# Kernel tuning notes

Hardware: AMD Instinct MI355X
Metric: run time of the kernel (lower is better)

Reference implementation:

```python
import jax, jax.numpy as jnp
import numpy as np

B = 262144
L, NO, NW = 5, 5, 3          # num_layers, num_ops, num_widths
AD = L * NO * NW             # arch_dim = 75
D, H = 64, 4                 # embed_dim, num_heads
HD = D // H                  # head_dim = 16
EPS = 1e-5


def _ln(x, g, b):
    m = x.mean(-1, keepdims=True)
    v = ((x - m) ** 2).mean(-1, keepdims=True)
    return (x - m) / jnp.sqrt(v + EPS) * g + b


def setup_inputs() -> dict:
    key = jax.random.key(0)
    ks = jax.random.split(key, 16)
    s = 0.05
    return {
        "hw_idx": jax.random.randint(ks[0], (B,), 0, 4),
        "op_indices": jax.random.randint(ks[1], (B, L), 0, NO),
        "width_indices": jax.random.randint(ks[2], (B, L), 0, NW),
        "hw_embed": jax.random.normal(ks[3], (4, D)) * s,
        "W1": jax.random.normal(ks[4], (128, AD)) * s, "b1": jnp.zeros((128,)),
        "W2": jax.random.normal(ks[5], (D, 128)) * s, "b2": jnp.zeros((D,)),
        "ln1_g": jnp.ones((D,)), "ln1_b": jnp.zeros((D,)),
        "in_proj_w": jax.random.normal(ks[6], (3 * D, D)) * s,
        "in_proj_b": jnp.zeros((3 * D,)),
        "out_proj_w": jax.random.normal(ks[7], (D, D)) * s,
        "out_proj_b": jnp.zeros((D,)),
        "ln2_g": jnp.ones((D,)), "ln2_b": jnp.zeros((D,)),
        "W3": jax.random.normal(ks[8], (32, D)) * s, "b3": jnp.zeros((32,)),
        "W4": jax.random.normal(ks[9], (1, 32)) * s, "b4": jnp.zeros((1,)),
    }


def reference(hw_idx, op_indices, width_indices, hw_embed, W1, b1, W2, b2,
              ln1_g, ln1_b, in_proj_w, in_proj_b, out_proj_w, out_proj_b,
              ln2_g, ln2_b, W3, b3, W4, b4):
    # hardware embedding lookup -> [B, D]
    hw_emb = hw_embed[hw_idx]
    # vectorized one-hot arch encoding: [B, L*NO*NW]
    cell = op_indices * NW + width_indices                  # [B, L]
    onehot = jax.nn.one_hot(cell, NO * NW, dtype=jnp.float32).reshape(-1, AD)
    # arch encoder MLP + LayerNorm (dropout = identity at eval)
    h = jax.nn.relu(onehot @ W1.T + b1)
    arch_emb = _ln(h @ W2.T + b2, ln1_g, ln1_b)             # [B, D]
    # combined sequence of 2 tokens: [B, 2, D]
    combined = jnp.stack([hw_emb, arch_emb], axis=1)
    # multi-head self-attention (torch MultiheadAttention, batch_first)
    qkv = combined @ in_proj_w.T + in_proj_b                # [B, 2, 3D]
    q, k, v = jnp.split(qkv, 3, axis=-1)
    q = q.reshape(-1, 2, H, HD); k = k.reshape(-1, 2, H, HD); v = v.reshape(-1, 2, H, HD)
    scores = jnp.einsum('bqhd,bkhd->bhqk', q, k) / np.sqrt(HD)
    attn = jax.nn.softmax(scores, axis=-1)
    ctx = jnp.einsum('bhqk,bkhd->bqhd', attn, v).reshape(-1, 2, D)
    attn_out = ctx @ out_proj_w.T + out_proj_b
    # residual + LayerNorm, mean-pool over the 2 tokens
    x = _ln(attn_out + combined, ln2_g, ln2_b)
    pooled = x.mean(axis=1)                                 # [B, D]
    # prediction head
    latency = jax.nn.relu(pooled @ W3.T + b3) @ W4.T + b4   # [B, 1]
    return latency
```

## Files before the change

kernel.cpp:

```cpp
#include <hip/hip_runtime.h>


using s8v = __attribute__((ext_vector_type(8))) short;
using h8  = __attribute__((ext_vector_type(8))) _Float16;
using h2v = __attribute__((ext_vector_type(2))) _Float16;
using f4  = __attribute__((ext_vector_type(4))) float;

#define WF_W1   0
#define WF_W2   12288
#define WF_IP   20480
#define WF_OP   32768
#define WF_W3   36864
#define WF_HWE  38912
#define TQ0     39168
#define TK0     39424
#define TV0B    39680
#define TV0R    39936
#define TBQ     40192

#define PWS     3456

__device__ __forceinline__ unsigned short f2h(float f) {
  _Float16 h = (_Float16)f;
  return __builtin_bit_cast(unsigned short, h);
}

__device__ __forceinline__ float dot8(h8 a, h8 b, float acc) {
  const f4 af = __builtin_bit_cast(f4, a), bf = __builtin_bit_cast(f4, b);
#pragma unroll
  for (int u = 0; u < 4; ++u)
    acc = __builtin_amdgcn_fdot2(__builtin_bit_cast(h2v, af[u]),
                                 __builtin_bit_cast(h2v, bf[u]), acc, false);
  return acc;
}

__device__ __forceinline__ void swz(const float* __restrict__ W,
                                    const float* __restrict__ bias,
                                    unsigned short* __restrict__ dst,
                                    int Kreal, int KS, int NT, int t, int stride) {
  const int total = KS * NT * 512;
  for (int i = t; i < total; i += stride) {
    const int j = i & 7, ln = (i >> 3) & 63, fr = i >> 9;
    const int nt = fr % NT, ks = fr / NT;
    const int n = nt * 16 + (ln & 15);
    const int k = ks * 32 + (ln >> 4) * 8 + j;
    float v = 0.f;
    if (k < Kreal) v = W[n * Kreal + k];
    else if (bias && k == Kreal) v = bias[n];
    dst[i] = f2h(v);
  }
}

__global__ void k_pre(const float* __restrict__ hwe,
                      const float* __restrict__ W1, const float* __restrict__ b1,
                      const float* __restrict__ W2,
                      const float* __restrict__ ipw, const float* __restrict__ ipb,
                      const float* __restrict__ opw,
                      const float* __restrict__ W3,
                      unsigned short* __restrict__ ws) {
  const int t = blockIdx.x * 256 + threadIdx.x;
  const int stride = gridDim.x * 256;
  swz(W1,  b1,      ws + WF_W1, 75, 3, 8, t, stride);
  swz(W2,  nullptr, ws + WF_W2, 128, 4, 4, t, stride);
  swz(ipw, nullptr, ws + WF_IP, 64, 2, 12, t, stride);
  swz(opw, nullptr, ws + WF_OP, 64, 2, 4, t, stride);
  swz(W3,  nullptr, ws + WF_W3, 64, 2, 2, t, stride);
  for (int i = t; i < 256; i += stride) ws[WF_HWE + i] = f2h(hwe[i]);
  for (int i = t; i < 768; i += stride) {
    const int hw = i / 192, n = i - hw * 192;
    const float* er = hwe + hw * 64;
    const float* wr = ipw + (size_t)n * 64;
    float acc = 0.f;
#pragma unroll 8
    for (int d = 0; d < 64; ++d) acc += er[d] * wr[d];
    if (n < 64)       ws[TQ0  + hw * 64 + n]         = f2h(acc + ipb[n]);
    else if (n < 128) ws[TK0  + hw * 64 + (n - 64)]  = f2h(acc);
    else {            ws[TV0B + hw * 64 + (n - 128)] = f2h(acc + ipb[n]);
                      ws[TV0R + hw * 64 + (n - 128)] = f2h(acc); }
  }
  for (int i = t; i < 64; i += stride) ws[TBQ + i] = f2h(ipb[i]);
}

__global__ __launch_bounds__(256, 4) void k_fused(
    const int* __restrict__ g_hw,
    const int* __restrict__ g_op, const int* __restrict__ g_wd,
    const float* __restrict__ g_hwe,
    const float* __restrict__ g_b2,
    const float* __restrict__ g_ln1g, const float* __restrict__ g_ln1b,
    const float* __restrict__ g_opb,
    const float* __restrict__ g_ln2g, const float* __restrict__ g_ln2b,
    const float* __restrict__ g_b3,  const float* __restrict__ g_W4,
    const float* __restrict__ g_b4,
    const unsigned short* __restrict__ wsf,
    float* __restrict__ g_out) {
  __shared__ __align__(16) unsigned short sm[4 * PWS];
  const int tid = threadIdx.x;
  const int wave = tid >> 6, lane = tid & 63;
  const int quad = lane >> 4, l15 = lane & 15;
  unsigned short* pw = sm + wave * PWS;
  const int m0 = (blockIdx.x * 4 + wave) * 16;

  int hwv = 0, c0 = 0, c1 = 0, c2 = 0, c3 = 0, c4 = 0;
  if (lane < 16) {
    const int smp = m0 + lane;
    hwv = g_hw[smp];
    c0 =      g_op[smp * 5 + 0] * 3 + g_wd[smp * 5 + 0];
    c1 = 15 + g_op[smp * 5 + 1] * 3 + g_wd[smp * 5 + 1];
    c2 = 30 + g_op[smp * 5 + 2] * 3 + g_wd[smp * 5 + 2];
    c3 = 45 + g_op[smp * 5 + 3] * 3 + g_wd[smp * 5 + 3];
    c4 = 60 + g_op[smp * 5 + 4] * 3 + g_wd[smp * 5 + 4];
  }
  const int t0 = __shfl(c0, l15), t1 = __shfl(c1, l15), t2 = __shfl(c2, l15);
  const int t3 = __shfl(c3, l15), t4 = __shfl(c4, l15);
  const int hwrow = __shfl(hwv, l15);

  float b2v[4], l1gv[4], l1bv[4], opbv[4], l2gv[4], l2bv[4];
#pragma unroll
  for (int nt = 0; nt < 4; ++nt) {
    const int col = nt * 16 + l15;
    b2v[nt] = g_b2[col];  l1gv[nt] = g_ln1g[col]; l1bv[nt] = g_ln1b[col];
    opbv[nt] = g_opb[col]; l2gv[nt] = g_ln2g[col]; l2bv[nt] = g_ln2b[col];
  }
  float b3v[2], w4vv[2];
#pragma unroll
  for (int nt = 0; nt < 2; ++nt) {
    b3v[nt] = g_b3[nt * 16 + l15];
    w4vv[nt] = g_W4[nt * 16 + l15];
  }
  const float b4v = g_b4[0];

  unsigned w0 = (1u << t0) | (1u << t1);
  unsigned w1 = 1u << (t3 - 32);
  unsigned w2 = 1u << 11;
  {
    const unsigned m2 = 1u << (t2 & 31);
    w0 |= (t2 < 32) ? m2 : 0u;
    w1 |= (t2 >= 32) ? m2 : 0u;
    const unsigned m4 = 1u << (t4 & 31);
    w1 |= (t4 < 64) ? m4 : 0u;
    w2 |= (t4 >= 64) ? m4 : 0u;
  }
  h8 aoh[3];
#pragma unroll
  for (int ks = 0; ks < 3; ++ks) {
    const unsigned wm = (ks == 0) ? w0 : (ks == 1) ? w1 : w2;
    const unsigned sh = wm >> (quad * 8);
    s8v a;
#pragma unroll
    for (int j = 0; j < 8; ++j)
      a[j] = ((sh >> j) & 1u) ? (short)0x3C00 : (short)0;
    aoh[ks] = __builtin_bit_cast(h8, a);
  }

#pragma unroll
  for (int half = 0; half < 2; ++half) {
    h8 bf[12];
#pragma unroll
    for (int n2 = 0; n2 < 4; ++n2)
#pragma unroll
      for (int ks = 0; ks < 3; ++ks)
        bf[n2 * 3 + ks] = *(const h8*)(wsf + WF_W1 +
            ((ks * 8 + half * 4 + n2) * 64 + lane) * 8);
#pragma unroll
    for (int n2 = 0; n2 < 4; ++n2) {
      f4 acc = {0.f, 0.f, 0.f, 0.f};
#pragma unroll
      for (int ks = 0; ks < 3; ++ks)
        acc = __builtin_amdgcn_mfma_f32_16x16x32_f16(aoh[ks], bf[n2 * 3 + ks],
                                                     acc, 0, 0, 0);
      const int col = (half * 4 + n2) * 16 + l15;
#pragma unroll
      for (int r = 0; r < 4; ++r) {
        float v = acc[r];
        v = v > 0.f ? v : 0.f;
        pw[(quad * 4 + r) * 136 + col] = f2h(v);
      }
    }
  }

  h8 a2[4];
#pragma unroll
  for (int ks = 0; ks < 4; ++ks)
    a2[ks] = *(const h8*)(pw + l15 * 136 + ks * 32 + quad * 8);
  float archres[4][4];
  {
    float val[4][4];
#pragma unroll
    for (int half = 0; half < 2; ++half) {
      h8 bf[8];
#pragma unroll
      for (int n2 = 0; n2 < 2; ++n2)
#pragma unroll
        for (int ks = 0; ks < 4; ++ks)
          bf[n2 * 4 + ks] = *(const h8*)(wsf + WF_W2 +
              ((ks * 4 + half * 2 + n2) * 64 + lane) * 8);
#pragma unroll
      for (int n2 = 0; n2 < 2; ++n2) {
        f4 acc = {0.f, 0.f, 0.f, 0.f};
#pragma unroll
        for (int ks = 0; ks < 4; ++ks)
          acc = __builtin_amdgcn_mfma_f32_16x16x32_f16(a2[ks], bf[n2 * 4 + ks],
                                                       acc, 0, 0, 0);
        const int nt = half * 2 + n2;
#pragma unroll
        for (int r = 0; r < 4; ++r) val[nt][r] = acc[r] + b2v[nt];
      }
    }
#pragma unroll
    for (int r = 0; r < 4; ++r) {
      float s = val[0][r] + val[1][r] + val[2][r] + val[3][r];
      float q = val[0][r] * val[0][r] + val[1][r] * val[1][r] +
                val[2][r] * val[2][r] + val[3][r] * val[3][r];
#pragma unroll
      for (int off = 1; off <= 8; off <<= 1) {
        s += __shfl_xor(s, off);
        q += __shfl_xor(q, off);
      }
      const float mean = s * (1.f / 64.f);
      const float var  = q * (1.f / 64.f) - mean * mean;
      const float rstd = rsqrtf(var + 1e-5f);
#pragma unroll
      for (int nt = 0; nt < 4; ++nt) {
        const int col = nt * 16 + l15;
        const float xn = (val[nt][r] - mean) * rstd * l1gv[nt] + l1bv[nt];
        archres[nt][r] = xn;
        pw[(quad * 4 + r) * 72 + col] = f2h(xn);
      }
    }
  }

  h8 at1[2];
#pragma unroll
  for (int ks = 0; ks < 2; ++ks)
    at1[ks] = *(const h8*)(pw + l15 * 72 + ks * 32 + quad * 8);
#pragma unroll
  for (int hh = 0; hh < 2; ++hh) {
    h8 bf[12];
#pragma unroll
    for (int h2 = 0; h2 < 2; ++h2) {
      const int h = hh * 2 + h2;
#pragma unroll
      for (int ks = 0; ks < 2; ++ks) {
        bf[h2 * 6 + 0 + ks] = *(const h8*)(wsf + WF_IP + ((ks * 12 + h    ) * 64 + lane) * 8);
        bf[h2 * 6 + 2 + ks] = *(const h8*)(wsf + WF_IP + ((ks * 12 + h + 4) * 64 + lane) * 8);
        bf[h2 * 6 + 4 + ks] = *(const h8*)(wsf + WF_IP + ((ks * 12 + h + 8) * 64 + lane) * 8);
      }
    }
#pragma unroll
    for (int h2 = 0; h2 < 2; ++h2) {
      const int h = hh * 2 + h2;
      f4 aq = {0.f,0.f,0.f,0.f}, ak = {0.f,0.f,0.f,0.f}, av = {0.f,0.f,0.f,0.f};
#pragma unroll
      for (int ks = 0; ks < 2; ++ks) {
        aq = __builtin_amdgcn_mfma_f32_16x16x32_f16(at1[ks], bf[h2 * 6 + 0 + ks], aq, 0, 0, 0);
        ak = __builtin_amdgcn_mfma_f32_16x16x32_f16(at1[ks], bf[h2 * 6 + 2 + ks], ak, 0, 0, 0);
        av = __builtin_amdgcn_mfma_f32_16x16x32_f16(at1[ks], bf[h2 * 6 + 4 + ks], av, 0, 0, 0);
      }
      const int col = h * 16 + l15;
#pragma unroll
      for (int r = 0; r < 4; ++r) {
        const int row = quad * 4 + r;
        pw[row * 72 + col]        = f2h(aq[r]);
        pw[1152 + row * 72 + col] = f2h(ak[r]);
        pw[2304 + row * 72 + col] = f2h(av[r]);
      }
    }
  }

  {
    const int qb = quad * 16;
    const unsigned short* q1p = pw + l15 * 72 + qb;
    const h8 q1a = *(const h8*)(q1p),          q1b = *(const h8*)(q1p + 8);
    const h8 k1a = *(const h8*)(q1p + 1152),   k1b = *(const h8*)(q1p + 1160);
    const h8 v1a = *(const h8*)(q1p + 2304),   v1b = *(const h8*)(q1p + 2312);
    const int tb = hwrow * 64 + qb;
    const h8 Q0a = *(const h8*)(wsf + TQ0 + tb),  Q0b = *(const h8*)(wsf + TQ0 + tb + 8);
    const h8 K0a = *(const h8*)(wsf + TK0 + tb),  K0b = *(const h8*)(wsf + TK0 + tb + 8);
    const h8 VBa = *(const h8*)(wsf + TV0B + tb), VBb = *(const h8*)(wsf + TV0B + tb + 8);
    const h8 VRa = *(const h8*)(wsf + TV0R + tb), VRb = *(const h8*)(wsf + TV0R + tb + 8);
    const h8 bqa = *(const h8*)(wsf + TBQ + qb),  bqb = *(const h8*)(wsf + TBQ + qb + 8);
    const h8 dka = k1a - K0a, dkb = k1b - K0b;
    const float d0 = dot8(Q0a, dka, dot8(Q0b, dkb, 0.f));
    const float d1 = dot8(q1a, dka, dot8(q1b, dkb,
                     dot8(bqa, dka, dot8(bqb, dkb, 0.f))));
    const float a01 = 1.f / (1.f + __expf(-d0 * 0.25f));
    const float a11 = 1.f / (1.f + __expf(-d1 * 0.25f));
    const h8 dva = v1a - VRa, dvb = v1b - VRb;
    h8 c0a, c0b, c1a, c1b;
#pragma unroll
    for (int j = 0; j < 8; ++j) {
      const float vb0 = (float)VBa[j], dv0 = (float)dva[j];
      const float vb1 = (float)VBb[j], dv1 = (float)dvb[j];
      c0a[j] = (_Float16)(vb0 + a01 * dv0);
      c0b[j] = (_Float16)(vb1 + a01 * dv1);
      c1a[j] = (_Float16)(vb0 + a11 * dv0);
      c1b[j] = (_Float16)(vb1 + a11 * dv1);
    }
    *(h8*)(pw + l15 * 72 + qb)            = c0a;
    *(h8*)(pw + l15 * 72 + qb + 8)        = c0b;
    *(h8*)(pw + (16 + l15) * 72 + qb)     = c1a;
    *(h8*)(pw + (16 + l15) * 72 + qb + 8) = c1b;
  }

  h8 ca[2][2];
#pragma unroll
  for (int mt = 0; mt < 2; ++mt)
#pragma unroll
    for (int ks = 0; ks < 2; ++ks)
      ca[mt][ks] = *(const h8*)(pw + (mt * 16 + l15) * 72 + ks * 32 + quad * 8);
  f4 oacc[2][4];
  {
    h8 bf[8];
#pragma unroll
    for (int nt = 0; nt < 4; ++nt)
#pragma unroll
      for (int ks = 0; ks < 2; ++ks)
        bf[nt * 2 + ks] = *(const h8*)(wsf + WF_OP + ((ks * 4 + nt) * 64 + lane) * 8);
#pragma unroll
    for (int nt = 0; nt < 4; ++nt)
#pragma unroll
      for (int mt = 0; mt < 2; ++mt) {
        f4 acc = {0.f, 0.f, 0.f, 0.f};
        acc = __builtin_amdgcn_mfma_f32_16x16x32_f16(ca[mt][0], bf[nt * 2 + 0], acc, 0, 0, 0);
        acc = __builtin_amdgcn_mfma_f32_16x16x32_f16(ca[mt][1], bf[nt * 2 + 1], acc, 0, 0, 0);
        oacc[mt][nt] = acc;
      }
  }
  float pool[4][4];
#pragma unroll
  for (int mt = 0; mt < 2; ++mt) {
    float val[4][4];
#pragma unroll
    for (int r = 0; r < 4; ++r) {
      if (mt == 0) {
        const int hr = __shfl(hwv, quad * 4 + r);
#pragma unroll
        for (int nt = 0; nt < 4; ++nt)
          val[nt][r] = oacc[0][nt][r] + opbv[nt] + g_hwe[hr * 64 + nt * 16 + l15];
      } else {
#pragma unroll
        for (int nt = 0; nt < 4; ++nt)
          val[nt][r] = oacc[1][nt][r] + opbv[nt] + archres[nt][r];
      }
    }
#pragma unroll
    for (int r = 0; r < 4; ++r) {
      float s = val[0][r] + val[1][r] + val[2][r] + val[3][r];
      float q = val[0][r] * val[0][r] + val[1][r] * val[1][r] +
                val[2][r] * val[2][r] + val[3][r] * val[3][r];
#pragma unroll
      for (int off = 1; off <= 8; off <<= 1) {
        s += __shfl_xor(s, off);
        q += __shfl_xor(q, off);
      }
      const float mean = s * (1.f / 64.f);
      const float var  = q * (1.f / 64.f) - mean * mean;
      const float rstd = rsqrtf(var + 1e-5f);
#pragma unroll
      for (int nt = 0; nt < 4; ++nt) {
        const float xn = (val[nt][r] - mean) * rstd * l2gv[nt] + l2bv[nt];
        if (mt == 0) pool[nt][r] = 0.5f * xn;
        else         pool[nt][r] += 0.5f * xn;
      }
    }
  }
#pragma unroll
  for (int nt = 0; nt < 4; ++nt)
#pragma unroll
    for (int r = 0; r < 4; ++r)
      pw[(quad * 4 + r) * 72 + nt * 16 + l15] = f2h(pool[nt][r]);

  h8 pa[2];
#pragma unroll
  for (int ks = 0; ks < 2; ++ks)
    pa[ks] = *(const h8*)(pw + l15 * 72 + ks * 32 + quad * 8);
  float part[4] = {0.f, 0.f, 0.f, 0.f};
  {
    h8 bf[4];
#pragma unroll
    for (int nt = 0; nt < 2; ++nt)
#pragma unroll
      for (int ks = 0; ks < 2; ++ks)
        bf[nt * 2 + ks] = *(const h8*)(wsf + WF_W3 + ((ks * 2 + nt) * 64 + lane) * 8);
#pragma unroll
    for (int nt = 0; nt < 2; ++nt) {
      f4 acc = {0.f, 0.f, 0.f, 0.f};
      acc = __builtin_amdgcn_mfma_f32_16x16x32_f16(pa[0], bf[nt * 2 + 0], acc, 0, 0, 0);
      acc = __builtin_amdgcn_mfma_f32_16x16x32_f16(pa[1], bf[nt * 2 + 1], acc, 0, 0, 0);
#pragma unroll
      for (int r = 0; r < 4; ++r) {
        float y = acc[r] + b3v[nt];
        y = y > 0.f ? y : 0.f;
        part[r] += y * w4vv[nt];
      }
    }
  }
#pragma unroll
  for (int off = 1; off <= 8; off <<= 1)
#pragma unroll
    for (int r = 0; r < 4; ++r)
      part[r] += __shfl_xor(part[r], off);
  if (l15 == 0) {
#pragma unroll
    for (int r = 0; r < 4; ++r)
      g_out[m0 + quad * 4 + r] = part[r] + b4v;
  }
}

extern "C" void kernel_launch(void* const* d_in, const int* in_sizes, int n_in,
                              void* d_out, int out_size, void* d_ws, size_t ws_size,
                              hipStream_t stream) {
  (void)in_sizes; (void)n_in; (void)out_size; (void)ws_size;
  unsigned short* ws = (unsigned short*)d_ws;

  k_pre<<<64, 256, 0, stream>>>(
      (const float*)d_in[3], (const float*)d_in[4], (const float*)d_in[5],
      (const float*)d_in[6], (const float*)d_in[10], (const float*)d_in[11],
      (const float*)d_in[12], (const float*)d_in[16], ws);

  k_fused<<<4096, 256, 0, stream>>>(
      (const int*)d_in[0],
      (const int*)d_in[1], (const int*)d_in[2],
      (const float*)d_in[3],
      (const float*)d_in[7],
      (const float*)d_in[8], (const float*)d_in[9],
      (const float*)d_in[13],
      (const float*)d_in[14], (const float*)d_in[15],
      (const float*)d_in[17], (const float*)d_in[18],
      (const float*)d_in[19],
      ws, (float*)d_out);
}
```

Baseline: 166.4 us.

## Stage per-layer weight fragments into shared LDS before each MFMA stage

Each block now cooperatively copies the pre-swizzled weight fragments for W1, W2, in_proj, and out_proj plus W3 from global memory into a shared LDS scratch region. All four waves then read their MFMA B operands from LDS instead of each wave fetching them from global. The goal is to cut redundant per-wave global and cache traffic for the weights. In exchange it adds many block-wide barriers and enlarges LDS use to about 52KB per block, which can lower occupancy and serialize the waves.

New measurement: 176.9 us. 1.06x slower.

```diff
diff --git a/kernel.cpp b/kernel.cpp
--- a/kernel.cpp
+++ b/kernel.cpp
@@ -18,6 +18,7 @@
 #define TV0R    39936
 #define TBQ     40192
 
+#define SCR     12288
 #define PWS     3456
 
 __device__ __forceinline__ unsigned short f2h(float f) {
@@ -32,6 +33,14 @@
     acc = __builtin_amdgcn_fdot2(__builtin_bit_cast(h2v, af[u]),
                                  __builtin_bit_cast(h2v, bf[u]), acc, false);
   return acc;
+}
+
+__device__ __forceinline__ void stage(const unsigned short* __restrict__ src,
+                                      unsigned short* __restrict__ dst,
+                                      int nf4, int tid) {
+  const f4* s = (const f4*)src;
+  f4* d = (f4*)dst;
+  for (int i = tid; i < nf4; i += 256) d[i] = s[i];
 }
 
 __device__ __forceinline__ void swz(const float* __restrict__ W,
@@ -93,12 +102,14 @@
     const float* __restrict__ g_b4,
     const unsigned short* __restrict__ wsf,
     float* __restrict__ g_out) {
-  __shared__ __align__(16) unsigned short sm[4 * PWS];
+  __shared__ __align__(16) unsigned short sm[SCR + 4 * PWS];
   const int tid = threadIdx.x;
   const int wave = tid >> 6, lane = tid & 63;
   const int quad = lane >> 4, l15 = lane & 15;
-  unsigned short* pw = sm + wave * PWS;
+  unsigned short* pw = sm + SCR + wave * PWS;
   const int m0 = (blockIdx.x * 4 + wave) * 16;
+
+  stage(wsf + WF_W1, sm, 1536, tid);
 
   int hwv = 0, c0 = 0, c1 = 0, c2 = 0, c3 = 0, c4 = 0;
   if (lane < 16) {
@@ -152,6 +163,8 @@
     aoh[ks] = __builtin_bit_cast(h8, a);
   }
 
+  __syncthreads();
+
 #pragma unroll
   for (int half = 0; half < 2; ++half) {
     h8 bf[12];
@@ -159,7 +172,7 @@
     for (int n2 = 0; n2 < 4; ++n2)
 #pragma unroll
       for (int ks = 0; ks < 3; ++ks)
-        bf[n2 * 3 + ks] = *(const h8*)(wsf + WF_W1 +
+        bf[n2 * 3 + ks] = *(const h8*)(sm +
             ((ks * 8 + half * 4 + n2) * 64 + lane) * 8);
 #pragma unroll
     for (int n2 = 0; n2 < 4; ++n2) {
@@ -178,10 +191,16 @@
     }
   }
 
+  __syncthreads();
+  stage(wsf + WF_W2, sm, 1024, tid);
+
   h8 a2[4];
 #pragma unroll
   for (int ks = 0; ks < 4; ++ks)
     a2[ks] = *(const h8*)(pw + l15 * 136 + ks * 32 + quad * 8);
+
+  __syncthreads();
+
   float archres[4][4];
   {
     float val[4][4];
@@ -192,7 +211,7 @@
       for (int n2 = 0; n2 < 2; ++n2)
 #pragma unroll
         for (int ks = 0; ks < 4; ++ks)
-          bf[n2 * 4 + ks] = *(const h8*)(wsf + WF_W2 +
+          bf[n2 * 4 + ks] = *(const h8*)(sm +
               ((ks * 4 + half * 2 + n2) * 64 + lane) * 8);
 #pragma unroll
       for (int n2 = 0; n2 < 2; ++n2) {
@@ -229,10 +248,16 @@
     }
   }
 
+  __syncthreads();
+  stage(wsf + WF_IP, sm, 1536, tid);
+
   h8 at1[2];
 #pragma unroll
   for (int ks = 0; ks < 2; ++ks)
     at1[ks] = *(const h8*)(pw + l15 * 72 + ks * 32 + quad * 8);
+
+  __syncthreads();
+
 #pragma unroll
   for (int hh = 0; hh < 2; ++hh) {
     h8 bf[12];
@@ -241,9 +266,9 @@
       const int h = hh * 2 + h2;
 #pragma unroll
       for (int ks = 0; ks < 2; ++ks) {
-        bf[h2 * 6 + 0 + ks] = *(const h8*)(wsf + WF_IP + ((ks * 12 + h    ) * 64 + lane) * 8);
-        bf[h2 * 6 + 2 + ks] = *(const h8*)(wsf + WF_IP + ((ks * 12 + h + 4) * 64 + lane) * 8);
-        bf[h2 * 6 + 4 + ks] = *(const h8*)(wsf + WF_IP + ((ks * 12 + h + 8) * 64 + lane) * 8);
+        bf[h2 * 6 + 0 + ks] = *(const h8*)(sm + ((ks * 12 + h    ) * 64 + lane) * 8);
+        bf[h2 * 6 + 2 + ks] = *(const h8*)(sm + ((ks * 12 + h + 4) * 64 + lane) * 8);
+        bf[h2 * 6 + 4 + ks] = *(const h8*)(sm + ((ks * 12 + h + 8) * 64 + lane) * 8);
       }
     }
 #pragma unroll
@@ -302,12 +327,18 @@
     *(h8*)(pw + (16 + l15) * 72 + qb + 8) = c1b;
   }
 
+  __syncthreads();
+  stage(wsf + WF_OP, sm, 768, tid);
+
   h8 ca[2][2];
 #pragma unroll
   for (int mt = 0; mt < 2; ++mt)
 #pragma unroll
     for (int ks = 0; ks < 2; ++ks)
       ca[mt][ks] = *(const h8*)(pw + (mt * 16 + l15) * 72 + ks * 32 + quad * 8);
+
+  __syncthreads();
+
   f4 oacc[2][4];
   {
     h8 bf[8];
@@ -315,7 +346,7 @@
     for (int nt = 0; nt < 4; ++nt)
 #pragma unroll
       for (int ks = 0; ks < 2; ++ks)
-        bf[nt * 2 + ks] = *(const h8*)(wsf + WF_OP + ((ks * 4 + nt) * 64 + lane) * 8);
+        bf[nt * 2 + ks] = *(const h8*)(sm + ((ks * 4 + nt) * 64 + lane) * 8);
 #pragma unroll
     for (int nt = 0; nt < 4; ++nt)
 #pragma unroll
@@ -381,7 +412,7 @@
     for (int nt = 0; nt < 2; ++nt)
 #pragma unroll
       for (int ks = 0; ks < 2; ++ks)
-        bf[nt * 2 + ks] = *(const h8*)(wsf + WF_W3 + ((ks * 2 + nt) * 64 + lane) * 8);
+        bf[nt * 2 + ks] = *(const h8*)(sm + 4096 + ((ks * 2 + nt) * 64 + lane) * 8);
 #pragma unroll
     for (int nt = 0; nt < 2; ++nt) {
       f4 acc = {0.f, 0.f, 0.f, 0.f};
```

## Process two 16-row tiles per wave to reuse weight fragments

Applied to the files above, without the earlier changes.

Each wave now handles 32 samples as two 16-row tiles, A and B, and shares every weight fragment loaded from global memory across both tiles' MFMAs. Blocks drop to 128 threads with launch bounds (128,2), and the grid stays at 4096 blocks, which still covers the full batch. The goal is to halve weight-fragment loads per sample and give the MFMA pipeline two independent accumulation chains. In exchange, register pressure rises with two sets of fragments and LayerNorm values, LDS per wave doubles, and fewer waves may be resident.

New measurement: 163.6 us. About the same (-1.7%).

```diff
diff --git a/kernel.cpp b/kernel.cpp
--- a/kernel.cpp
+++ b/kernel.cpp
@@ -19,6 +19,7 @@
 #define TBQ     40192
 
 #define PWS     3456
+#define WPS     6912
 
 __device__ __forceinline__ unsigned short f2h(float f) {
   _Float16 h = (_Float16)f;
@@ -81,7 +82,7 @@
   for (int i = t; i < 64; i += stride) ws[TBQ + i] = f2h(ipb[i]);
 }
 
-__global__ __launch_bounds__(256, 4) void k_fused(
+__global__ __launch_bounds__(128, 2) void k_fused(
     const int* __restrict__ g_hw,
     const int* __restrict__ g_op, const int* __restrict__ g_wd,
     const float* __restrict__ g_hwe,
@@ -93,15 +94,16 @@
     const float* __restrict__ g_b4,
     const unsigned short* __restrict__ wsf,
     float* __restrict__ g_out) {
-  __shared__ __align__(16) unsigned short sm[4 * PWS];
+  __shared__ __align__(16) unsigned short sm[2 * WPS];
   const int tid = threadIdx.x;
   const int wave = tid >> 6, lane = tid & 63;
   const int quad = lane >> 4, l15 = lane & 15;
-  unsigned short* pw = sm + wave * PWS;
-  const int m0 = (blockIdx.x * 4 + wave) * 16;
+  unsigned short* pwA = sm + wave * WPS;
+  unsigned short* pwB = pwA + PWS;
+  const int m0 = (blockIdx.x * 2 + wave) * 32;
 
   int hwv = 0, c0 = 0, c1 = 0, c2 = 0, c3 = 0, c4 = 0;
-  if (lane < 16) {
+  if (lane < 32) {
     const int smp = m0 + lane;
     hwv = g_hw[smp];
     c0 =      g_op[smp * 5 + 0] * 3 + g_wd[smp * 5 + 0];
@@ -110,9 +112,12 @@
     c3 = 45 + g_op[smp * 5 + 3] * 3 + g_wd[smp * 5 + 3];
     c4 = 60 + g_op[smp * 5 + 4] * 3 + g_wd[smp * 5 + 4];
   }
-  const int t0 = __shfl(c0, l15), t1 = __shfl(c1, l15), t2 = __shfl(c2, l15);
-  const int t3 = __shfl(c3, l15), t4 = __shfl(c4, l15);
-  const int hwrow = __shfl(hwv, l15);
+  const int tA0 = __shfl(c0, l15), tA1 = __shfl(c1, l15), tA2 = __shfl(c2, l15);
+  const int tA3 = __shfl(c3, l15), tA4 = __shfl(c4, l15);
+  const int tB0 = __shfl(c0, 16 + l15), tB1 = __shfl(c1, 16 + l15);
+  const int tB2 = __shfl(c2, 16 + l15), tB3 = __shfl(c3, 16 + l15);
+  const int tB4 = __shfl(c4, 16 + l15);
+  const int hwrowA = __shfl(hwv, l15), hwrowB = __shfl(hwv, 16 + l15);
 
   float b2v[4], l1gv[4], l1bv[4], opbv[4], l2gv[4], l2bv[4];
 #pragma unroll
@@ -129,27 +134,36 @@
   }
   const float b4v = g_b4[0];
 
-  unsigned w0 = (1u << t0) | (1u << t1);
-  unsigned w1 = 1u << (t3 - 32);
-  unsigned w2 = 1u << 11;
+  h8 aohA[3], aohB[3];
   {
-    const unsigned m2 = 1u << (t2 & 31);
-    w0 |= (t2 < 32) ? m2 : 0u;
-    w1 |= (t2 >= 32) ? m2 : 0u;
-    const unsigned m4 = 1u << (t4 & 31);
-    w1 |= (t4 < 64) ? m4 : 0u;
-    w2 |= (t4 >= 64) ? m4 : 0u;
-  }
-  h8 aoh[3];
-#pragma unroll
-  for (int ks = 0; ks < 3; ++ks) {
-    const unsigned wm = (ks == 0) ? w0 : (ks == 1) ? w1 : w2;
-    const unsigned sh = wm >> (quad * 8);
-    s8v a;
-#pragma unroll
-    for (int j = 0; j < 8; ++j)
-      a[j] = ((sh >> j) & 1u) ? (short)0x3C00 : (short)0;
-    aoh[ks] = __builtin_bit_cast(h8, a);
+    unsigned wa0 = (1u << tA0) | (1u << tA1);
+    unsigned wa1 = 1u << (tA3 - 32);
+    unsigned wa2 = 1u << 11;
+    const unsigned ma2 = 1u << (tA2 & 31);
+    wa0 |= (tA2 < 32) ? ma2 : 0u;  wa1 |= (tA2 >= 32) ? ma2 : 0u;
+    const unsigned ma4 = 1u << (tA4 & 31);
+    wa1 |= (tA4 < 64) ? ma4 : 0u;  wa2 |= (tA4 >= 64) ? ma4 : 0u;
+    unsigned wb0 = (1u << tB0) | (1u << tB1);
+    unsigned wb1 = 1u << (tB3 - 32);
+    unsigned wb2 = 1u << 11;
+    const unsigned mb2 = 1u << (tB2 & 31);
+    wb0 |= (tB2 < 32) ? mb2 : 0u;  wb1 |= (tB2 >= 32) ? mb2 : 0u;
+    const unsigned mb4 = 1u << (tB4 & 31);
+    wb1 |= (tB4 < 64) ? mb4 : 0u;  wb2 |= (tB4 >= 64) ? mb4 : 0u;
+#pragma unroll
+    for (int ks = 0; ks < 3; ++ks) {
+      const unsigned wma = (ks == 0) ? wa0 : (ks == 1) ? wa1 : wa2;
+      const unsigned wmb = (ks == 0) ? wb0 : (ks == 1) ? wb1 : wb2;
+      const unsigned sa = wma >> (quad * 8), sb = wmb >> (quad * 8);
+      s8v a, b;
+#pragma unroll
+      for (int j = 0; j < 8; ++j) {
+        a[j] = ((sa >> j) & 1u) ? (short)0x3C00 : (short)0;
+        b[j] = ((sb >> j) & 1u) ? (short)0x3C00 : (short)0;
+      }
+      aohA[ks] = __builtin_bit_cast(h8, a);
+      aohB[ks] = __builtin_bit_cast(h8, b);
+    }
   }
 
 #pragma unroll
@@ -163,28 +177,32 @@
             ((ks * 8 + half * 4 + n2) * 64 + lane) * 8);
 #pragma unroll
     for (int n2 = 0; n2 < 4; ++n2) {
-      f4 acc = {0.f, 0.f, 0.f, 0.f};
-#pragma unroll
-      for (int ks = 0; ks < 3; ++ks)
-        acc = __builtin_amdgcn_mfma_f32_16x16x32_f16(aoh[ks], bf[n2 * 3 + ks],
-                                                     acc, 0, 0, 0);
+      f4 accA = {0.f, 0.f, 0.f, 0.f}, accB = {0.f, 0.f, 0.f, 0.f};
+#pragma unroll
+      for (int ks = 0; ks < 3; ++ks) {
+        accA = __builtin_amdgcn_mfma_f32_16x16x32_f16(aohA[ks], bf[n2 * 3 + ks], accA, 0, 0, 0);
+        accB = __builtin_amdgcn_mfma_f32_16x16x32_f16(aohB[ks], bf[n2 * 3 + ks], accB, 0, 0, 0);
+      }
       const int col = (half * 4 + n2) * 16 + l15;
 #pragma unroll
       for (int r = 0; r < 4; ++r) {
-        float v = acc[r];
-        v = v > 0.f ? v : 0.f;
-        pw[(quad * 4 + r) * 136 + col] = f2h(v);
-      }
-    }
-  }
-
-  h8 a2[4];
-#pragma unroll
-  for (int ks = 0; ks < 4; ++ks)
-    a2[ks] = *(const h8*)(pw + l15 * 136 + ks * 32 + quad * 8);
-  float archres[4][4];
+        const float vA = accA[r] > 0.f ? accA[r] : 0.f;
+        const float vB = accB[r] > 0.f ? accB[r] : 0.f;
+        pwA[(quad * 4 + r) * 136 + col] = f2h(vA);
+        pwB[(quad * 4 + r) * 136 + col] = f2h(vB);
+      }
+    }
+  }
+
+  h8 a2A[4], a2B[4];
+#pragma unroll
+  for (int ks = 0; ks < 4; ++ks) {
+    a2A[ks] = *(const h8*)(pwA + l15 * 136 + ks * 32 + quad * 8);
+    a2B[ks] = *(const h8*)(pwB + l15 * 136 + ks * 32 + quad * 8);
+  }
+  float archresA[4][4], archresB[4][4];
   {
-    float val[4][4];
+    float valA[4][4], valB[4][4];
 #pragma unroll
     for (int half = 0; half < 2; ++half) {
       h8 bf[8];
@@ -196,43 +214,56 @@
               ((ks * 4 + half * 2 + n2) * 64 + lane) * 8);
 #pragma unroll
       for (int n2 = 0; n2 < 2; ++n2) {
-        f4 acc = {0.f, 0.f, 0.f, 0.f};
-#pragma unroll
-        for (int ks = 0; ks < 4; ++ks)
-          acc = __builtin_amdgcn_mfma_f32_16x16x32_f16(a2[ks], bf[n2 * 4 + ks],
-                                                       acc, 0, 0, 0);
+        f4 accA = {0.f, 0.f, 0.f, 0.f}, accB = {0.f, 0.f, 0.f, 0.f};
+#pragma unroll
+        for (int ks = 0; ks < 4; ++ks) {
+          accA = __builtin_amdgcn_mfma_f32_16x16x32_f16(a2A[ks], bf[n2 * 4 + ks], accA, 0, 0, 0);
+          accB = __builtin_amdgcn_mfma_f32_16x16x32_f16(a2B[ks], bf[n2 * 4 + ks], accB, 0, 0, 0);
+        }
         const int nt = half * 2 + n2;
 #pragma unroll
-        for (int r = 0; r < 4; ++r) val[nt][r] = acc[r] + b2v[nt];
+        for (int r = 0; r < 4; ++r) {
+          valA[nt][r] = accA[r] + b2v[nt];
+          valB[nt][r] = accB[r] + b2v[nt];
+        }
       }
     }
 #pragma unroll
     for (int r = 0; r < 4; ++r) {
-      float s = val[0][r] + val[1][r] + val[2][r] + val[3][r];
-      float q = val[0][r] * val[0][r] + val[1][r] * val[1][r] +
-                val[2][r] * val[2][r] + val[3][r] * val[3][r];
+      float sA = valA[0][r] + valA[1][r] + valA[2][r] + valA[3][r];
+      float qA = valA[0][r] * valA[0][r] + valA[1][r] * valA[1][r] +
+                 valA[2][r] * valA[2][r] + valA[3][r] * valA[3][r];
+      float sB = valB[0][r] + valB[1][r] + valB[2][r] + valB[3][r];
+      float qB = valB[0][r] * valB[0][r] + valB[1][r] * valB[1][r] +
+                 valB[2][r] * valB[2][r] + valB[3][r] * valB[3][r];
 #pragma unroll
       for (int off = 1; off <= 8; off <<= 1) {
-        s += __shfl_xor(s, off);
-        q += __shfl_xor(q, off);
-      }
-      const float mean = s * (1.f / 64.f);
-      const float var  = q * (1.f / 64.f) - mean * mean;
-      const float rstd = rsqrtf(var + 1e-5f);
+        sA += __shfl_xor(sA, off);  qA += __shfl_xor(qA, off);
+        sB += __shfl_xor(sB, off);  qB += __shfl_xor(qB, off);
+      }
+      const float meanA = sA * (1.f / 64.f);
+      const float rstdA = rsqrtf(qA * (1.f / 64.f) - meanA * meanA + 1e-5f);
+      const float meanB = sB * (1.f / 64.f);
+      const float rstdB = rsqrtf(qB * (1.f / 64.f) - meanB * meanB + 1e-5f);
 #pragma unroll
       for (int nt = 0; nt < 4; ++nt) {
         const int col = nt * 16 + l15;
-        const float xn = (val[nt][r] - mean) * rstd * l1gv[nt] + l1bv[nt];
-        archres[nt][r] = xn;
-        pw[(quad * 4 + r) * 72 + col] = f2h(xn);
-      }
-    }
-  }
-
-  h8 at1[2];
-#pragma unroll
-  for (int ks = 0; ks < 2; ++ks)
-    at1[ks] = *(const h8*)(pw + l15 * 72 + ks * 32 + quad * 8);
+        const float xnA = (valA[nt][r] - meanA) * rstdA * l1gv[nt] + l1bv[nt];
+        const float xnB = (valB[nt][r] - meanB) * rstdB * l1gv[nt] + l1bv[nt];
+        archresA[nt][r] = xnA;
+        archresB[nt][r] = xnB;
+        pwA[(quad * 4 + r) * 72 + col] = f2h(xnA);
+        pwB[(quad * 4 + r) * 72 + col] = f2h(xnB);
+      }
+    }
+  }
+
+  h8 at1A[2], at1B[2];
+#pragma unroll
+  for (int ks = 0; ks < 2; ++ks) {
+    at1A[ks] = *(const h8*)(pwA + l15 * 72 + ks * 32 + quad * 8);
+    at1B[ks] = *(const h8*)(pwB + l15 * 72 + ks * 32 + quad * 8);
+  }
 #pragma unroll
   for (int hh = 0; hh < 2; ++hh) {
     h8 bf[12];
@@ -249,25 +280,35 @@
 #pragma unroll
     for (int h2 = 0; h2 < 2; ++h2) {
       const int h = hh * 2 + h2;
-      f4 aq = {0.f,0.f,0.f,0.f}, ak = {0.f,0.f,0.f,0.f}, av = {0.f,0.f,0.f,0.f};
+      f4 aqA = {0.f,0.f,0.f,0.f}, akA = {0.f,0.f,0.f,0.f}, avA = {0.f,0.f,0.f,0.f};
+      f4 aqB = {0.f,0.f,0.f,0.f}, akB = {0.f,0.f,0.f,0.f}, avB = {0.f,0.f,0.f,0.f};
 #pragma unroll
       for (int ks = 0; ks < 2; ++ks) {
-        aq = __builtin_amdgcn_mfma_f32_16x16x32_f16(at1[ks], bf[h2 * 6 + 0 + ks], aq, 0, 0, 0);
-        ak = __builtin_amdgcn_mfma_f32_16x16x32_f16(at1[ks], bf[h2 * 6 + 2 + ks], ak, 0, 0, 0);
-        av = __builtin_amdgcn_mfma_f32_16x16x32_f16(at1[ks], bf[h2 * 6 + 4 + ks], av, 0, 0, 0);
+        aqA = __builtin_amdgcn_mfma_f32_16x16x32_f16(at1A[ks], bf[h2 * 6 + 0 + ks], aqA, 0, 0, 0);
+        akA = __builtin_amdgcn_mfma_f32_16x16x32_f16(at1A[ks], bf[h2 * 6 + 2 + ks], akA, 0, 0, 0);
+        avA = __builtin_amdgcn_mfma_f32_16x16x32_f16(at1A[ks], bf[h2 * 6 + 4 + ks], avA, 0, 0, 0);
+        aqB = __builtin_amdgcn_mfma_f32_16x16x32_f16(at1B[ks], bf[h2 * 6 + 0 + ks], aqB, 0, 0, 0);
+        akB = __builtin_amdgcn_mfma_f32_16x16x32_f16(at1B[ks], bf[h2 * 6 + 2 + ks], akB, 0, 0, 0);
+        avB = __builtin_amdgcn_mfma_f32_16x16x32_f16(at1B[ks], bf[h2 * 6 + 4 + ks], avB, 0, 0, 0);
       }
       const int col = h * 16 + l15;
 #pragma unroll
       for (int r = 0; r < 4; ++r) {
         const int row = quad * 4 + r;
-        pw[row * 72 + col]        = f2h(aq[r]);
-        pw[1152 + row * 72 + col] = f2h(ak[r]);
-        pw[2304 + row * 72 + col] = f2h(av[r]);
-      }
-    }
-  }
-
-  {
+        pwA[row * 72 + col]        = f2h(aqA[r]);
+        pwA[1152 + row * 72 + col] = f2h(akA[r]);
+        pwA[2304 + row * 72 + col] = f2h(avA[r]);
+        pwB[row * 72 + col]        = f2h(aqB[r]);
+        pwB[1152 + row * 72 + col] = f2h(akB[r]);
+        pwB[2304 + row * 72 + col] = f2h(avB[r]);
+      }
+    }
+  }
+
+#pragma unroll
+  for (int tile = 0; tile < 2; ++tile) {
+    unsigned short* pw = tile ? pwB : pwA;
+    const int hwrow = tile ? hwrowB : hwrowA;
     const int qb = quad * 16;
     const unsigned short* q1p = pw + l15 * 72 + qb;
     const h8 q1a = *(const h8*)(q1p),          q1b = *(const h8*)(q1p + 8);
@@ -302,13 +343,6 @@
     *(h8*)(pw + (16 + l15) * 72 + qb + 8) = c1b;
   }
 
-  h8 ca[2][2];
-#pragma unroll
-  for (int mt = 0; mt < 2; ++mt)
-#pragma unroll
-    for (int ks = 0; ks < 2; ++ks)
-      ca[mt][ks] = *(const h8*)(pw + (mt * 16 + l15) * 72 + ks * 32 + quad * 8);
-  f4 oacc[2][4];
   {
     h8 bf[8];
 #pragma unroll
@@ -317,64 +351,71 @@
       for (int ks = 0; ks < 2; ++ks)
         bf[nt * 2 + ks] = *(const h8*)(wsf + WF_OP + ((ks * 4 + nt) * 64 + lane) * 8);
 #pragma unroll
-    for (int nt = 0; nt < 4; ++nt)
+    for (int tile = 0; tile < 2; ++tile) {
+      unsigned short* pw = tile ? pwB : pwA;
+      h8 ca[2][2];
+#pragma unroll
+      for (int mt = 0; mt < 2; ++mt)
+#pragma unroll
+        for (int ks = 0; ks < 2; ++ks)
+          ca[mt][ks] = *(const h8*)(pw + (mt * 16 + l15) * 72 + ks * 32 + quad * 8);
+      f4 oacc[2][4];
+#pragma unroll
+      for (int nt = 0; nt < 4; ++nt)
+#pragma unroll
+        for (int mt = 0; mt < 2; ++mt) {
+          f4 acc = {0.f, 0.f, 0.f, 0.f};
+          acc = __builtin_amdgcn_mfma_f32_16x16x32_f16(ca[mt][0], bf[nt * 2 + 0], acc, 0, 0, 0);
+          acc = __builtin_amdgcn_mfma_f32_16x16x32_f16(ca[mt][1], bf[nt * 2 + 1], acc, 0, 0, 0);
+          oacc[mt][nt] = acc;
+        }
+      float pool[4][4];
 #pragma unroll
       for (int mt = 0; mt < 2; ++mt) {
-        f4 acc = {0.f, 0.f, 0.f, 0.f};
-        acc = __builtin_amdgcn_mfma_f32_16x16x32_f16(ca[mt][0], bf[nt * 2 + 0], acc, 0, 0, 0);
-        acc = __builtin_amdgcn_mfma_f32_16x16x32_f16(ca[mt][1], bf[nt * 2 + 1], acc, 0, 0, 0);
-        oacc[mt][nt] = acc;
-      }
-  }
-  float pool[4][4];
-#pragma unroll
-  for (int mt = 0; mt < 2; ++mt) {
-    float val[4][4];
-#pragma unroll
-    for (int r = 0; r < 4; ++r) {
-      if (mt == 0) {
-        const int hr = __shfl(hwv, quad * 4 + r);
-#pragma unroll
-        for (int nt = 0; nt < 4; ++nt)
-          val[nt][r] = oacc[0][nt][r] + opbv[nt] + g_hwe[hr * 64 + nt * 16 + l15];
-      } else {
-#pragma unroll
-        for (int nt = 0; nt < 4; ++nt)
-          val[nt][r] = oacc[1][nt][r] + opbv[nt] + archres[nt][r];
-      }
-    }
-#pragma unroll
-    for (int r = 0; r < 4; ++r) {
-      float s = val[0][r] + val[1][r] + val[2][r] + val[3][r];
-      float q = val[0][r] * val[0][r] + val[1][r] * val[1][r] +
-                val[2][r] * val[2][r] + val[3][r] * val[3][r];
-#pragma unroll
-      for (int off = 1; off <= 8; off <<= 1) {
-        s += __shfl_xor(s, off);
-        q += __shfl_xor(q, off);
-      }
-      const float mean = s * (1.f / 64.f);
-      const float var  = q * (1.f / 64.f) - mean * mean;
-      const float rstd = rsqrtf(var + 1e-5f);
-#pragma unroll
-      for (int nt = 0; nt < 4; ++nt) {
-        const float xn = (val[nt][r] - mean) * rstd * l2gv[nt] + l2bv[nt];
-        if (mt == 0) pool[nt][r] = 0.5f * xn;
-        else         pool[nt][r] += 0.5f * xn;
-      }
-    }
-  }
-#pragma unroll
-  for (int nt = 0; nt < 4; ++nt)
-#pragma unroll
-    for (int r = 0; r < 4; ++r)
-      pw[(quad * 4 + r) * 72 + nt * 16 + l15] = f2h(pool[nt][r]);
-
-  h8 pa[2];
-#pragma unroll
-  for (int ks = 0; ks < 2; ++ks)
-    pa[ks] = *(const h8*)(pw + l15 * 72 + ks * 32 + quad * 8);
-  float part[4] = {0.f, 0.f, 0.f, 0.f};
+        float val[4][4];
+#pragma unroll
+        for (int r = 0; r < 4; ++r) {
+          if (mt == 0) {
+            const int hr = __shfl(hwv, tile * 16 + quad * 4 + r);
+#pragma unroll
+            for (int nt = 0; nt < 4; ++nt)
+              val[nt][r] = oacc[0][nt][r] + opbv[nt] + g_hwe[hr * 64 + nt * 16 + l15];
+          } else {
+#pragma unroll
+            for (int nt = 0; nt < 4; ++nt)
+              val[nt][r] = oacc[1][nt][r] + opbv[nt] +
+                           (tile ? archresB[nt][r] : archresA[nt][r]);
+          }
+        }
+#pragma unroll
+        for (int r = 0; r < 4; ++r) {
+          float s = val[0][r] + val[1][r] + val[2][r] + val[3][r];
+          float q = val[0][r] * val[0][r] + val[1][r] * val[1][r] +
+                    val[2][r] * val[2][r] + val[3][r] * val[3][r];
+#pragma unroll
+          for (int off = 1; off <= 8; off <<= 1) {
+            s += __shfl_xor(s, off);
+            q += __shfl_xor(q, off);
+          }
+          const float mean = s * (1.f / 64.f);
+          const float var  = q * (1.f / 64.f) - mean * mean;
+          const float rstd = rsqrtf(var + 1e-5f);
+#pragma unroll
+          for (int nt = 0; nt < 4; ++nt) {
+            const float xn = (val[nt][r] - mean) * rstd * l2gv[nt] + l2bv[nt];
+            if (mt == 0) pool[nt][r] = 0.5f * xn;
+            else         pool[nt][r] += 0.5f * xn;
+          }
+        }
+      }
+#pragma unroll
+      for (int nt = 0; nt < 4; ++nt)
+#pragma unroll
+        for (int r = 0; r < 4; ++r)
+          pw[(quad * 4 + r) * 72 + nt * 16 + l15] = f2h(pool[nt][r]);
+    }
+  }
+
   {
     h8 bf[4];
 #pragma unroll
@@ -383,27 +424,36 @@
       for (int ks = 0; ks < 2; ++ks)
         bf[nt * 2 + ks] = *(const h8*)(wsf + WF_W3 + ((ks * 2 + nt) * 64 + lane) * 8);
 #pragma unroll
-    for (int nt = 0; nt < 2; ++nt) {
-      f4 acc = {0.f, 0.f, 0.f, 0.f};
-      acc = __builtin_amdgcn_mfma_f32_16x16x32_f16(pa[0], bf[nt * 2 + 0], acc, 0, 0, 0);
-      acc = __builtin_amdgcn_mfma_f32_16x16x32_f16(pa[1], bf[nt * 2 + 1], acc, 0, 0, 0);
-#pragma unroll
-      for (int r = 0; r < 4; ++r) {
-        float y = acc[r] + b3v[nt];
-        y = y > 0.f ? y : 0.f;
-        part[r] += y * w4vv[nt];
-      }
-    }
-  }
-#pragma unroll
-  for (int off = 1; off <= 8; off <<= 1)
-#pragma unroll
-    for (int r = 0; r < 4; ++r)
-      part[r] += __shfl_xor(part[r], off);
-  if (l15 == 0) {
-#pragma unroll
-    for (int r = 0; r < 4; ++r)
-      g_out[m0 + quad * 4 + r] = part[r] + b4v;
+    for (int tile = 0; tile < 2; ++tile) {
+      unsigned short* pw = tile ? pwB : pwA;
+      h8 pa[2];
+#pragma unroll
+      for (int ks = 0; ks < 2; ++ks)
+        pa[ks] = *(const h8*)(pw + l15 * 72 + ks * 32 + quad * 8);
+      float part[4] = {0.f, 0.f, 0.f, 0.f};
+#pragma unroll
+      for (int nt = 0; nt < 2; ++nt) {
+        f4 acc = {0.f, 0.f, 0.f, 0.f};
+        acc = __builtin_amdgcn_mfma_f32_16x16x32_f16(pa[0], bf[nt * 2 + 0], acc, 0, 0, 0);
+        acc = __builtin_amdgcn_mfma_f32_16x16x32_f16(pa[1], bf[nt * 2 + 1], acc, 0, 0, 0);
+#pragma unroll
+        for (int r = 0; r < 4; ++r) {
+          float y = acc[r] + b3v[nt];
+          y = y > 0.f ? y : 0.f;
+          part[r] += y * w4vv[nt];
+        }
+      }
+#pragma unroll
+      for (int off = 1; off <= 8; off <<= 1)
+#pragma unroll
+        for (int r = 0; r < 4; ++r)
+          part[r] += __shfl_xor(part[r], off);
+      if (l15 == 0) {
+#pragma unroll
+        for (int r = 0; r < 4; ++r)
+          g_out[m0 + tile * 16 + quad * 4 + r] = part[r] + b4v;
+      }
+    }
   }
 }
 
@@ -418,7 +468,7 @@
       (const float*)d_in[6], (const float*)d_in[10], (const float*)d_in[11],
       (const float*)d_in[12], (const float*)d_in[16], ws);
 
-  k_fused<<<4096, 256, 0, stream>>>(
+  k_fused<<<4096, 128, 0, stream>>>(
       (const int*)d_in[0],
       (const int*)d_in[1], (const int*)d_in[2],
       (const float*)d_in[3],
```
